# Kernel optimization log

Measured on AMD Instinct MI355X. Metric: run time of the kernel, lower is better.

## Reference

```python
import jax, jax.numpy as jnp
import numpy as np

# static config (levels=4, CDA=False branch -> self_attn_4, scale=4, f=False)
SHAPES = [(80, 80), (40, 40), (20, 20), (10, 10)]
D = 256; NH = 8; NL = 4; NP = 4; DFF = 1024; DH = D // NH
L = sum(h * w for h, w in SHAPES)  # 8500
B = 1


def layer_norm(x, g, b, eps=1e-5):
    m = jnp.mean(x, axis=-1, keepdims=True)
    v = jnp.mean((x - m) ** 2, axis=-1, keepdims=True)
    return (x - m) * jax.lax.rsqrt(v + eps) * g + b


def ms_deform_attn_core(value, loc, attn):
    # value: [B, L, NH, DH]; loc: [B, Lq, NH, NL, NP, 2] in [0,1]; attn: [B, Lq, NH, NL, NP]
    Bq, Lq = loc.shape[0], loc.shape[1]
    out = jnp.zeros((Bq, NH, Lq, DH), value.dtype)
    start = 0
    for lvl, (Hl, Wl) in enumerate(SHAPES):
        v = value[:, start:start + Hl * Wl]          # [B, HW, NH, DH]
        start += Hl * Wl
        v = v.transpose(0, 2, 1, 3)                  # [B, NH, HW, DH]
        ll = loc[:, :, :, lvl]                       # [B, Lq, NH, NP, 2]
        # grid_sample semantics: align_corners=False, padding_mode='zeros'
        x = ll[..., 0] * Wl - 0.5
        y = ll[..., 1] * Hl - 0.5
        x0 = jnp.floor(x); y0 = jnp.floor(y)
        acc = jnp.zeros((Bq, NH, Lq, NP, DH), value.dtype)
        for dy in (0, 1):
            for dx in (0, 1):
                xi = x0 + dx; yi = y0 + dy
                w = (1.0 - jnp.abs(x - xi)) * (1.0 - jnp.abs(y - yi))  # [B,Lq,NH,NP]
                valid = (xi >= 0) & (xi < Wl) & (yi >= 0) & (yi < Hl)
                xi_c = jnp.clip(xi, 0, Wl - 1).astype(jnp.int32)
                yi_c = jnp.clip(yi, 0, Hl - 1).astype(jnp.int32)
                lin = (yi_c * Wl + xi_c).transpose(0, 2, 1, 3).reshape(Bq, NH, Lq * NP)
                g = jnp.take_along_axis(v, lin[..., None], axis=2).reshape(Bq, NH, Lq, NP, DH)
                wv = (w * valid.astype(w.dtype)).transpose(0, 2, 1, 3)[..., None]
                acc = acc + g * wv
        aw = attn[:, :, :, lvl].transpose(0, 2, 1, 3)[..., None]  # [B,NH,Lq,NP,1]
        out = out + jnp.sum(acc * aw, axis=3)
    return out.transpose(0, 2, 1, 3).reshape(Bq, Lq, NH * DH)


def setup_inputs():
    key = jax.random.key(0)
    ks = jax.random.split(key, 24)
    s = 0.02
    d = {}
    d['src'] = jax.random.normal(ks[0], (B, L, D), jnp.float32)
    d['pos'] = jax.random.normal(ks[1], (B, L, D), jnp.float32)
    d['reference_points'] = jax.random.uniform(ks[2], (B, L, NL, 2), jnp.float32)
    d['spatial_shapes'] = jnp.array(SHAPES, jnp.int32)
    d['level_start_index'] = jnp.array(np.cumsum([0] + [h * w for h, w in SHAPES[:-1]]), jnp.int32)
    d['scale'] = 4
    # MSDeformAttn params
    d['Wo'] = jax.random.normal(ks[3], (D, NH * NL * NP * 2), jnp.float32) * s
    d['bo'] = jax.random.normal(ks[4], (NH * NL * NP * 2,), jnp.float32) * s
    d['Wa'] = jax.random.normal(ks[5], (D, NH * NL * NP), jnp.float32) * s
    d['ba'] = jax.random.normal(ks[6], (NH * NL * NP,), jnp.float32) * s
    d['Wv'] = jax.random.normal(ks[7], (D, D), jnp.float32) * s
    d['bv'] = jnp.zeros((D,), jnp.float32)
    d['Wout'] = jax.random.normal(ks[8], (D, D), jnp.float32) * s
    d['bout'] = jnp.zeros((D,), jnp.float32)
    # FFN + LayerNorms
    d['W1'] = jax.random.normal(ks[9], (D, DFF), jnp.float32) * s
    d['b1'] = jnp.zeros((DFF,), jnp.float32)
    d['W2'] = jax.random.normal(ks[10], (DFF, D), jnp.float32) * s
    d['b2'] = jnp.zeros((D,), jnp.float32)
    d['g1'] = jnp.ones((D,), jnp.float32); d['be1'] = jnp.zeros((D,), jnp.float32)
    d['g2'] = jnp.ones((D,), jnp.float32); d['be2'] = jnp.zeros((D,), jnp.float32)
    return d


def reference(src, pos, reference_points, spatial_shapes, level_start_index, scale,
              Wo, bo, Wa, ba, Wv, bv, Wout, bout, W1, b1, W2, b2, g1, be1, g2, be2):
    Bq, Lq, _ = src.shape
    q = src + pos  # with_pos_embed
    # sampling offsets & attention weights (softmax over levels*points)
    off = (q @ Wo + bo).reshape(Bq, Lq, NH, NL, NP, 2)
    attn = jax.nn.softmax((q @ Wa + ba).reshape(Bq, Lq, NH, NL * NP), axis=-1)
    attn = attn.reshape(Bq, Lq, NH, NL, NP)
    value = (src @ Wv + bv).reshape(Bq, L, NH, DH)
    # offset normalizer is (W, H) per level
    normalizer = jnp.stack([spatial_shapes[:, 1], spatial_shapes[:, 0]], -1).astype(src.dtype)
    loc = reference_points[:, :, None, :, None, :] + off / normalizer[None, None, None, :, None, :]
    src2 = ms_deform_attn_core(value, loc, attn) @ Wout + bout
    # residual + norm1 (dropout = eval identity)
    x = layer_norm(src + src2, g1, be1)
    # FFN
    ffn = jax.nn.relu(x @ W1 + b1) @ W2 + b2
    x = layer_norm(x + ffn, g2, be2)
    return x
```

## Files before the change

kernel.cpp:

```cpp
#include <hip/hip_runtime.h>
#include <hip/hip_bf16.h>
#include <string.h>

#define D 256
#define NH 8
#define DH 32
#define NL 4
#define NP 4
#define DFF 1024
#define LTOT 8500

typedef __bf16 bf16x8 __attribute__((ext_vector_type(8)));
typedef float floatx4 __attribute__((ext_vector_type(4)));

__device__ inline unsigned bpack(float a, float b) {
    __hip_bfloat16 ha = __float2bfloat16(a), hb = __float2bfloat16(b);
    unsigned short ua, ub;
    memcpy(&ua, &ha, 2); memcpy(&ub, &hb, 2);
    return (unsigned)ua | ((unsigned)ub << 16);
}

__device__ inline void gload16(const void* g, void* l) {
    __builtin_amdgcn_global_load_lds((const __attribute__((address_space(1))) void*)g,
                                     (__attribute__((address_space(3))) void*)l,
                                     16, 0, 0);
}

__global__ void transpose_all(const float* W0, const float* W1_, const float* W2_,
                              const float* W3, const float* W4, const float* W5,
                              __hip_bfloat16* T0, __hip_bfloat16* T1, __hip_bfloat16* T2,
                              __hip_bfloat16* T3, __hip_bfloat16* T4, __hip_bfloat16* T5,
                              const float* src, const float* pos,
                              __hip_bfloat16* qb, __hip_bfloat16* srcb) {
    int id = blockIdx.x;
    if (id >= 736) {
        int idx = (id - 736) * 2048 + threadIdx.x * 8;
        if (idx < LTOT * 256) {
            float4 s0 = *(const float4*)(src + idx);
            float4 s1 = *(const float4*)(src + idx + 4);
            float4 p0 = *(const float4*)(pos + idx);
            float4 p1 = *(const float4*)(pos + idx + 4);
            uint4 us, uq;
            us.x = bpack(s0.x, s0.y); us.y = bpack(s0.z, s0.w);
            us.z = bpack(s1.x, s1.y); us.w = bpack(s1.z, s1.w);
            uq.x = bpack(s0.x + p0.x, s0.y + p0.y); uq.y = bpack(s0.z + p0.z, s0.w + p0.w);
            uq.z = bpack(s1.x + p1.x, s1.y + p1.y); uq.w = bpack(s1.z + p1.z, s1.w + p1.w);
            *(uint4*)(srcb + idx) = us;
            *(uint4*)(qb + idx)  = uq;
        }
        return;
    }
    const int cum[7] = {0, 64, 96, 160, 224, 480, 736};
    int mi = 0;
    while (id >= cum[mi + 1]) mi++;
    int lid = id - cum[mi];
    const float* W; __hip_bfloat16* T; int K, N;
    switch (mi) {
        case 0: W = W0; T = T0; K = 256;  N = 256;  break;
        case 1: W = W1_; T = T1; K = 256; N = 128;  break;
        case 2: W = W2_; T = T2; K = 256; N = 256;  break;
        case 3: W = W3; T = T3; K = 256;  N = 256;  break;
        case 4: W = W4; T = T4; K = 256;  N = 1024; break;
        default: W = W5; T = T5; K = 1024; N = 256; break;
    }
    int ntx = N >> 5;
    int n0 = (lid % ntx) * 32, k0 = (lid / ntx) * 32;
    __shared__ float t[32][33];
    int tx = threadIdx.x & 31, ty = threadIdx.x >> 5;
#pragma unroll
    for (int i = 0; i < 32; i += 8)
        t[ty + i][tx] = W[(size_t)(k0 + ty + i) * N + n0 + tx];
    __syncthreads();
#pragma unroll
    for (int i = 0; i < 32; i += 8)
        T[(size_t)(n0 + ty + i) * K + k0 + tx] = __float2bfloat16(t[tx][ty + i]);
}

__global__ __launch_bounds__(256) void proj2(
    const __hip_bfloat16* __restrict__ qb, const __hip_bfloat16* __restrict__ srcb,
    const __hip_bfloat16* __restrict__ WoT, const __hip_bfloat16* __restrict__ WaT,
    const __hip_bfloat16* __restrict__ WvT,
    const float* __restrict__ bo, const float* __restrict__ ba, const float* __restrict__ bv,
    float* __restrict__ locb, float* __restrict__ attnb, __hip_bfloat16* __restrict__ valb,
    int M) {
    constexpr int BM = 64, BN = 64, BK = 64, K = 256;
    __shared__ __align__(16) __hip_bfloat16 sA[BM * BK];
    __shared__ __align__(16) __hip_bfloat16 sB[BN * BK];

    int n0 = blockIdx.x * BN;
    int m0 = blockIdx.y * BM;

    const __hip_bfloat16* BT;
    const __hip_bfloat16* A;
    const float* bias;
    int ncol0, Nout;
    float* Cf; __hip_bfloat16* Cb;
    if (n0 < 256)      { A = qb;   BT = WoT; bias = bo; ncol0 = n0;       Nout = 256; Cf = locb;  Cb = nullptr; }
    else if (n0 < 384) { A = qb;   BT = WaT; bias = ba; ncol0 = n0 - 256; Nout = 128; Cf = attnb; Cb = nullptr; }
    else               { A = srcb; BT = WvT; bias = bv; ncol0 = n0 - 384; Nout = 256; Cf = nullptr; Cb = valb; }

    int tid = threadIdx.x, wave = tid >> 6, lane = tid & 63;
    int wm = (wave >> 1) * 32, wn = (wave & 1) * 32;

    floatx4 acc[2][2];
#pragma unroll
    for (int i = 0; i < 2; i++)
#pragma unroll
        for (int j = 0; j < 2; j++)
#pragma unroll
            for (int e = 0; e < 4; e++) acc[i][j][e] = 0.f;

    int lrow = lane & 15, swz = lrow & 7;
    int scol = ((lane & 7) ^ (lane >> 3)) << 3;

    const __hip_bfloat16* aP[2];
    const __hip_bfloat16* bP[2];
#pragma unroll
    for (int i = 0; i < 2; i++) {
        int ra = m0 + i * 32 + wave * 8 + (lane >> 3); if (ra >= M) ra = M - 1;
        aP[i] = A + (size_t)ra * K + scol;
        int rb = ncol0 + i * 32 + wave * 8 + (lane >> 3);
        bP[i] = BT + (size_t)rb * K + scol;
    }
    int dOff = wave * 1024 + lane * 16;

    for (int k0 = 0; k0 < K; k0 += BK) {
#pragma unroll
        for (int i = 0; i < 2; i++) gload16(aP[i] + k0, (char*)sA + i * 4096 + dOff);
#pragma unroll
        for (int i = 0; i < 2; i++) gload16(bP[i] + k0, (char*)sB + i * 4096 + dOff);
        __syncthreads();
#pragma unroll
        for (int kk = 0; kk < 2; kk++) {
            int co = (((kk << 2) + (lane >> 4)) ^ swz) << 3;
            bf16x8 af[2], bfr[2];
#pragma unroll
            for (int tm = 0; tm < 2; tm++)
                af[tm] = *(const bf16x8*)(&sA[(wm + tm * 16 + lrow) * BK + co]);
#pragma unroll
            for (int tn = 0; tn < 2; tn++)
                bfr[tn] = *(const bf16x8*)(&sB[(wn + tn * 16 + lrow) * BK + co]);
#pragma unroll
            for (int tm = 0; tm < 2; tm++)
#pragma unroll
                for (int tn = 0; tn < 2; tn++)
                    acc[tm][tn] = __builtin_amdgcn_mfma_f32_16x16x32_bf16(af[tm], bfr[tn], acc[tm][tn], 0, 0, 0);
        }
        __syncthreads();
    }

    int lcol = lane & 15, lr4 = (lane >> 4) * 4;
#pragma unroll
    for (int tm = 0; tm < 2; tm++) {
#pragma unroll
        for (int i = 0; i < 4; i++) {
            int row = m0 + wm + tm * 16 + lr4 + i;
            if (row < M) {
#pragma unroll
                for (int tn = 0; tn < 2; tn++) {
                    int col = ncol0 + wn + tn * 16 + lcol;
                    float v = acc[tm][tn][i] + bias[col];
                    if (Cf) Cf[(size_t)row * Nout + col] = v;
                    else    Cb[(size_t)row * Nout + col] = __float2bfloat16(v);
                }
            }
        }
    }
}

__global__ __launch_bounds__(256) void deform(const __hip_bfloat16* __restrict__ value,
                                              const float* __restrict__ locraw,
                                              const float* __restrict__ logits,
                                              const float* __restrict__ refp,
                                              __hip_bfloat16* __restrict__ out) {
    __shared__ float wS[4][8][16][4];
    __shared__ int   aS[4][8][16][4];
    int tid = threadIdx.x;
    int q0 = blockIdx.x * 4;

    {
        int sub = tid >> 6, h = (tid >> 3) & 7, t8 = tid & 7;
        int q = q0 + sub;
        const float* lg = logits + q * 128 + h * 16;
        float l0 = lg[t8], l1 = lg[t8 + 8];
        float mx = fmaxf(l0, l1);
#pragma unroll
        for (int m = 1; m < 8; m <<= 1) mx = fmaxf(mx, __shfl_xor(mx, m, 64));
        float e0 = __expf(l0 - mx), e1 = __expf(l1 - mx);
        float s = e0 + e1;
#pragma unroll
        for (int m = 1; m < 8; m <<= 1) s += __shfl_xor(s, m, 64);
        float inv = 1.f / s;

        const int starts[4] = {0, 6400, 8000, 8400};
#pragma unroll
        for (int j = 0; j < 2; j++) {
            int pp = t8 + 8 * j;
            float a = (j ? e1 : e0) * inv;
            int l = pp >> 2;
            int Wl = 80 >> l;
            float nv = (float)Wl;
            float rx = refp[q * 8 + l * 2 + 0];
            float ry = refp[q * 8 + l * 2 + 1];
            float lx = rx + locraw[q * 256 + h * 32 + pp * 2 + 0] / nv;
            float ly = ry + locraw[q * 256 + h * 32 + pp * 2 + 1] / nv;
            float x = lx * nv - 0.5f;
            float y = ly * nv - 0.5f;
            float x0f = floorf(x), y0f = floorf(y);
            float fx = x - x0f, fy = y - y0f;
            int x0 = (int)x0f, y0 = (int)y0f;
            float wts[4] = {(1.f - fx) * (1.f - fy), fx * (1.f - fy),
                            (1.f - fx) * fy,         fx * fy};
            int st = starts[l];
#pragma unroll
            for (int t = 0; t < 4; t++) {
                int xi = x0 + (t & 1), yi = y0 + (t >> 1);
                bool valid = (xi >= 0) & (xi < Wl) & (yi >= 0) & (yi < Wl);
                int xc = min(max(xi, 0), Wl - 1), yc = min(max(yi, 0), Wl - 1);
                wS[sub][h][pp][t] = valid ? wts[t] * a : 0.f;
                aS[sub][h][pp][t] = (st + yc * Wl + xc) * 512 + h * 64;
            }
        }
    }
    __syncthreads();

    int sub = tid >> 6, h = (tid >> 3) & 7, l8 = tid & 7;
    int q = q0 + sub;
    const char* vb = (const char*)value;
    int lo = l8 * 8;
    float a0 = 0.f, a1 = 0.f, a2 = 0.f, a3 = 0.f;
#pragma unroll
    for (int p = 0; p < 16; p++) {
        floatx4 w = *(const floatx4*)&wS[sub][h][p][0];
        int4 av = *(const int4*)&aS[sub][h][p][0];
#pragma unroll
        for (int t = 0; t < 4; t++) {
            int ad = (t == 0) ? av.x : (t == 1) ? av.y : (t == 2) ? av.z : av.w;
            uint2 u = *(const uint2*)(vb + ad + lo);
            float wt = w[t];
            a0 += wt * __uint_as_float(u.x << 16);
            a1 += wt * __uint_as_float(u.x & 0xffff0000u);
            a2 += wt * __uint_as_float(u.y << 16);
            a3 += wt * __uint_as_float(u.y & 0xffff0000u);
        }
    }
    uint2 o;
    o.x = bpack(a0, a1);
    o.y = bpack(a2, a3);
    *(uint2*)((char*)out + q * 512 + h * 64 + l8 * 8) = o;
}

__global__ __launch_bounds__(512) void tail(
    const __hip_bfloat16* __restrict__ aob,
    const __hip_bfloat16* __restrict__ WoutT, const float* __restrict__ bout,
    const float* __restrict__ src,
    const float* __restrict__ g1, const float* __restrict__ be1,
    const __hip_bfloat16* __restrict__ W1T, const float* __restrict__ b1,
    const __hip_bfloat16* __restrict__ W2T, const float* __restrict__ b2,
    const float* __restrict__ g2, const float* __restrict__ be2,
    float* __restrict__ outf, int M) {
    __shared__ __align__(16) __hip_bfloat16 sAx[16 * 256];
    __shared__ __align__(16) __hip_bfloat16 H[16 * 1032];
    __shared__ __align__(16) __hip_bfloat16 sB[256 * 64];
    __shared__ float psum[8][16], psq[8][16], mS[16], rS[16];

    int tid = threadIdx.x, wave = tid >> 6, lane = tid & 63;
    int m0 = blockIdx.x * 16;
    int lrow = lane & 15, swz = lrow & 7, q2 = lane >> 4;
    int quad = lane >> 4, lcol = lane & 15;
    int swzA = (lrow & 7) << 3;
    int scolB = ((tid & 7) ^ ((tid >> 3) & 7)) << 3;

    {
        int rr = tid >> 5, cc = tid & 31;
        int gr = m0 + rr; if (gr >= M) gr = M - 1;
        int colel = (cc * 8) ^ ((rr & 7) << 3);
        gload16(aob + (size_t)gr * 256 + colel, (char*)sAx + tid * 16);
    }

    const __hip_bfloat16* bP[4];
#pragma unroll
    for (int i = 0; i < 4; i++)
        bP[i] = WoutT + (size_t)(i * 64 + (tid >> 3)) * 256 + scolB;

    floatx4 acc[2];
#pragma unroll
    for (int j = 0; j < 2; j++)
#pragma unroll
        for (int e = 0; e < 4; e++) acc[j][e] = 0.f;

    for (int t = 0; t < 4; t++) {
#pragma unroll
        for (int i = 0; i < 4; i++) gload16(bP[i] + t * 64, (char*)sB + i * 8192 + tid * 16);
        __syncthreads();
#pragma unroll
        for (int kk = 0; kk < 2; kk++) {
            int co = (((kk << 2) + q2) ^ swz) << 3;
            bf16x8 af = *(const bf16x8*)(&sAx[lrow * 256 + ((t * 64 + kk * 32 + q2 * 8) ^ swzA)]);
            bf16x8 bfr[2];
#pragma unroll
            for (int tn = 0; tn < 2; tn++)
                bfr[tn] = *(const bf16x8*)(&sB[(wave * 32 + tn * 16 + lrow) * 64 + co]);
#pragma unroll
            for (int tn = 0; tn < 2; tn++)
                acc[tn] = __builtin_amdgcn_mfma_f32_16x16x32_bf16(af, bfr[tn], acc[tn], 0, 0, 0);
        }
        __syncthreads();
    }

    float v1[2][4];
#pragma unroll
    for (int i = 0; i < 4; i++) {
        int row = quad * 4 + i;
        int grow = m0 + row; if (grow >= M) grow = M - 1;
#pragma unroll
        for (int tn = 0; tn < 2; tn++) {
            int col = wave * 32 + tn * 16 + lcol;
            v1[tn][i] = acc[tn][i] + bout[col] + src[(size_t)grow * 256 + col];
        }
    }
#pragma unroll
    for (int i = 0; i < 4; i++) {
        float s = 0.f, s2 = 0.f;
#pragma unroll
        for (int tn = 0; tn < 2; tn++) { float x = v1[tn][i]; s += x; s2 += x * x; }
#pragma unroll
        for (int m = 1; m < 16; m <<= 1) {
            s  += __shfl_xor(s, m, 64);
            s2 += __shfl_xor(s2, m, 64);
        }
        if (lcol == 0) { int row = quad * 4 + i; psum[wave][row] = s; psq[wave][row] = s2; }
    }
    __syncthreads();
    if (tid < 16) {
        float s = 0.f, s2 = 0.f;
#pragma unroll
        for (int w = 0; w < 8; w++) { s += psum[w][tid]; s2 += psq[w][tid]; }
        float m = s * (1.f / 256.f);
        float var = fmaxf(s2 * (1.f / 256.f) - m * m, 0.f);
        mS[tid] = m; rS[tid] = rsqrtf(var + 1e-5f);
    }
    __syncthreads();

    float x1r[2][4];
#pragma unroll
    for (int i = 0; i < 4; i++) {
        int row = quad * 4 + i;
        float m = mS[row], r = rS[row];
#pragma unroll
        for (int tn = 0; tn < 2; tn++) {
            int col = wave * 32 + tn * 16 + lcol;
            float o = (v1[tn][i] - m) * r * g1[col] + be1[col];
            x1r[tn][i] = o;
            sAx[row * 256 + (col ^ ((row & 7) << 3))] = __float2bfloat16(o);
        }
    }

    for (int c = 0; c < 4; c++) {
        const __hip_bfloat16* bPc[4];
#pragma unroll
        for (int i = 0; i < 4; i++)
            bPc[i] = W1T + (size_t)(c * 256 + i * 64 + (tid >> 3)) * 256 + scolB;

        floatx4 accA[2];
#pragma unroll
        for (int j = 0; j < 2; j++)
#pragma unroll
            for (int e = 0; e < 4; e++) accA[j][e] = 0.f;

        for (int t = 0; t < 4; t++) {
#pragma unroll
            for (int i = 0; i < 4; i++) gload16(bPc[i] + t * 64, (char*)sB + i * 8192 + tid * 16);
            __syncthreads();
#pragma unroll
            for (int kk = 0; kk < 2; kk++) {
                int co = (((kk << 2) + q2) ^ swz) << 3;
                bf16x8 af = *(const bf16x8*)(&sAx[lrow * 256 + ((t * 64 + kk * 32 + q2 * 8) ^ swzA)]);
                bf16x8 bfr[2];
#pragma unroll
                for (int tn = 0; tn < 2; tn++)
                    bfr[tn] = *(const bf16x8*)(&sB[(wave * 32 + tn * 16 + lrow) * 64 + co]);
#pragma unroll
                for (int tn = 0; tn < 2; tn++)
                    accA[tn] = __builtin_amdgcn_mfma_f32_16x16x32_bf16(af, bfr[tn], accA[tn], 0, 0, 0);
            }
            __syncthreads();
        }

#pragma unroll
        for (int i = 0; i < 4; i++) {
            int row = quad * 4 + i;
#pragma unroll
            for (int tn = 0; tn < 2; tn++) {
                int col = c * 256 + wave * 32 + tn * 16 + lcol;
                float v = accA[tn][i] + b1[col];
                H[row * 1032 + col] = __float2bfloat16(fmaxf(v, 0.f));
            }
        }
    }

    const __hip_bfloat16* bP2[4];
#pragma unroll
    for (int i = 0; i < 4; i++)
        bP2[i] = W2T + (size_t)(i * 64 + (tid >> 3)) * 1024 + scolB;

    floatx4 acc2[2];
#pragma unroll
    for (int j = 0; j < 2; j++)
#pragma unroll
        for (int e = 0; e < 4; e++) acc2[j][e] = 0.f;

    for (int t = 0; t < 16; t++) {
#pragma unroll
        for (int i = 0; i < 4; i++) gload16(bP2[i] + t * 64, (char*)sB + i * 8192 + tid * 16);
        __syncthreads();
#pragma unroll
        for (int kk = 0; kk < 2; kk++) {
            int co = (((kk << 2) + q2) ^ swz) << 3;
            bf16x8 af = *(const bf16x8*)(&H[lrow * 1032 + t * 64 + kk * 32 + q2 * 8]);
            bf16x8 bfr[2];
#pragma unroll
            for (int tn = 0; tn < 2; tn++)
                bfr[tn] = *(const bf16x8*)(&sB[(wave * 32 + tn * 16 + lrow) * 64 + co]);
#pragma unroll
            for (int tn = 0; tn < 2; tn++)
                acc2[tn] = __builtin_amdgcn_mfma_f32_16x16x32_bf16(af, bfr[tn], acc2[tn], 0, 0, 0);
        }
        __syncthreads();
    }

    float v2[2][4];
#pragma unroll
    for (int i = 0; i < 4; i++) {
#pragma unroll
        for (int tn = 0; tn < 2; tn++) {
            int col = wave * 32 + tn * 16 + lcol;
            v2[tn][i] = acc2[tn][i] + b2[col] + x1r[tn][i];
        }
    }
#pragma unroll
    for (int i = 0; i < 4; i++) {
        float s = 0.f, s2 = 0.f;
#pragma unroll
        for (int tn = 0; tn < 2; tn++) { float x = v2[tn][i]; s += x; s2 += x * x; }
#pragma unroll
        for (int m = 1; m < 16; m <<= 1) {
            s  += __shfl_xor(s, m, 64);
            s2 += __shfl_xor(s2, m, 64);
        }
        if (lcol == 0) { int row = quad * 4 + i; psum[wave][row] = s; psq[wave][row] = s2; }
    }
    __syncthreads();
    if (tid < 16) {
        float s = 0.f, s2 = 0.f;
#pragma unroll
        for (int w = 0; w < 8; w++) { s += psum[w][tid]; s2 += psq[w][tid]; }
        float m = s * (1.f / 256.f);
        float var = fmaxf(s2 * (1.f / 256.f) - m * m, 0.f);
        mS[tid] = m; rS[tid] = rsqrtf(var + 1e-5f);
    }
    __syncthreads();

#pragma unroll
    for (int i = 0; i < 4; i++) {
        int row = quad * 4 + i;
        int grow = m0 + row;
        if (grow < M) {
            float m = mS[row], r = rS[row];
#pragma unroll
            for (int tn = 0; tn < 2; tn++) {
                int col = wave * 32 + tn * 16 + lcol;
                outf[(size_t)grow * 256 + col] = (v2[tn][i] - m) * r * g2[col] + be2[col];
            }
        }
    }
}

extern "C" void kernel_launch(void* const* d_in, const int* in_sizes, int n_in,
                              void* d_out, int out_size, void* d_ws, size_t ws_size,
                              hipStream_t stream) {
    const float* src  = (const float*)d_in[0];
    const float* pos  = (const float*)d_in[1];
    const float* refp = (const float*)d_in[2];
    const float* Wo   = (const float*)d_in[6];
    const float* bo   = (const float*)d_in[7];
    const float* Wa   = (const float*)d_in[8];
    const float* ba   = (const float*)d_in[9];
    const float* Wv   = (const float*)d_in[10];
    const float* bv   = (const float*)d_in[11];
    const float* Wout = (const float*)d_in[12];
    const float* bout = (const float*)d_in[13];
    const float* W1   = (const float*)d_in[14];
    const float* b1   = (const float*)d_in[15];
    const float* W2   = (const float*)d_in[16];
    const float* b2   = (const float*)d_in[17];
    const float* g1   = (const float*)d_in[18];
    const float* be1  = (const float*)d_in[19];
    const float* g2   = (const float*)d_in[20];
    const float* be2  = (const float*)d_in[21];
    float* out = (float*)d_out;
    char* ws = (char*)d_ws;

    __hip_bfloat16* WoT   = (__hip_bfloat16*)(ws + 0);
    __hip_bfloat16* WaT   = (__hip_bfloat16*)(ws + 131072);
    __hip_bfloat16* WvT   = (__hip_bfloat16*)(ws + 196608);
    __hip_bfloat16* WoutT = (__hip_bfloat16*)(ws + 327680);
    __hip_bfloat16* W1T   = (__hip_bfloat16*)(ws + 458752);
    __hip_bfloat16* W2T   = (__hip_bfloat16*)(ws + 983040);
    float*          locb  = (float*)(ws + 1507328);
    float*          attnb = (float*)(ws + 10211328);
    __hip_bfloat16* valb  = (__hip_bfloat16*)(ws + 14563328);
    __hip_bfloat16* aob   = (__hip_bfloat16*)(ws + 18915328);
    __hip_bfloat16* qb    = (__hip_bfloat16*)(ws + 23267328);
    __hip_bfloat16* srcb  = (__hip_bfloat16*)(ws + 27619328);

    transpose_all<<<736 + 1063, 256, 0, stream>>>(Wo, Wa, Wv, Wout, W1, W2,
                                                  WoT, WaT, WvT, WoutT, W1T, W2T,
                                                  src, pos, qb, srcb);

    proj2<<<dim3(10, 133), 256, 0, stream>>>(qb, srcb, WoT, WaT, WvT, bo, ba, bv,
                                             locb, attnb, valb, LTOT);

    deform<<<2125, 256, 0, stream>>>(valb, locb, attnb, refp, aob);

    tail<<<532, 512, 0, stream>>>(aob, WoutT, bout, src, g1, be1,
                                  W1T, b1, W2T, b2, g2, be2, out, LTOT);
}
```

Before: 197.7 us.

## Defer tail weight transposes into deform kernel and widen proj2 K tile

The transposes of Wout, W1 and W2 move out of the first prep kernel and become 576 extra blocks appended to the deform kernel. This shortens the critical path before proj2 and lets that work overlap with the memory-bound gather. proj2 also doubles its K tile to 128 with a new 16-way XOR swizzle, halving the number of K iterations and barriers at the cost of doubled LDS per block. Deform now uses a 32KB shared buffer, which could lower occupancy for the gather blocks.

```diff
diff --git a/kernel.cpp b/kernel.cpp
--- a/kernel.cpp
+++ b/kernel.cpp
@@ -26,54 +26,48 @@
                                      16, 0, 0);
 }
 
-__global__ void transpose_all(const float* W0, const float* W1_, const float* W2_,
-                              const float* W3, const float* W4, const float* W5,
-                              __hip_bfloat16* T0, __hip_bfloat16* T1, __hip_bfloat16* T2,
-                              __hip_bfloat16* T3, __hip_bfloat16* T4, __hip_bfloat16* T5,
-                              const float* src, const float* pos,
-                              __hip_bfloat16* qb, __hip_bfloat16* srcb) {
+__device__ inline void wtile(const float* W, __hip_bfloat16* T, int K, int N,
+                             int n0, int k0, float* t ) {
+    int tx = threadIdx.x & 31, ty = threadIdx.x >> 5;
+#pragma unroll
+    for (int i = 0; i < 32; i += 8)
+        t[(ty + i) * 33 + tx] = W[(size_t)(k0 + ty + i) * N + n0 + tx];
+    __syncthreads();
+#pragma unroll
+    for (int i = 0; i < 32; i += 8)
+        T[(size_t)(n0 + ty + i) * K + k0 + tx] = __float2bfloat16(t[tx * 33 + ty + i]);
+    __syncthreads();
+}
+
+__global__ void prep3(const float* Wo, const float* Wa, const float* Wv,
+                      __hip_bfloat16* WoT, __hip_bfloat16* WaT, __hip_bfloat16* WvT,
+                      const float* src, const float* pos,
+                      __hip_bfloat16* qb, __hip_bfloat16* srcb) {
+    __shared__ float t[32 * 33];
     int id = blockIdx.x;
-    if (id >= 736) {
-        int idx = (id - 736) * 2048 + threadIdx.x * 8;
-        if (idx < LTOT * 256) {
-            float4 s0 = *(const float4*)(src + idx);
-            float4 s1 = *(const float4*)(src + idx + 4);
-            float4 p0 = *(const float4*)(pos + idx);
-            float4 p1 = *(const float4*)(pos + idx + 4);
-            uint4 us, uq;
-            us.x = bpack(s0.x, s0.y); us.y = bpack(s0.z, s0.w);
-            us.z = bpack(s1.x, s1.y); us.w = bpack(s1.z, s1.w);
-            uq.x = bpack(s0.x + p0.x, s0.y + p0.y); uq.y = bpack(s0.z + p0.z, s0.w + p0.w);
-            uq.z = bpack(s1.x + p1.x, s1.y + p1.y); uq.w = bpack(s1.z + p1.z, s1.w + p1.w);
-            *(uint4*)(srcb + idx) = us;
-            *(uint4*)(qb + idx)  = uq;
-        }
+    if (id < 160) {
+        const float* W; __hip_bfloat16* T; int K, N, lid;
+        if (id < 64)       { W = Wo; T = WoT; K = 256; N = 256; lid = id; }
+        else if (id < 96)  { W = Wa; T = WaT; K = 256; N = 128; lid = id - 64; }
+        else               { W = Wv; T = WvT; K = 256; N = 256; lid = id - 96; }
+        int ntx = N >> 5;
+        wtile(W, T, K, N, (lid % ntx) * 32, (lid / ntx) * 32, t);
         return;
     }
-    const int cum[7] = {0, 64, 96, 160, 224, 480, 736};
-    int mi = 0;
-    while (id >= cum[mi + 1]) mi++;
-    int lid = id - cum[mi];
-    const float* W; __hip_bfloat16* T; int K, N;
-    switch (mi) {
-        case 0: W = W0; T = T0; K = 256;  N = 256;  break;
-        case 1: W = W1_; T = T1; K = 256; N = 128;  break;
-        case 2: W = W2_; T = T2; K = 256; N = 256;  break;
-        case 3: W = W3; T = T3; K = 256;  N = 256;  break;
-        case 4: W = W4; T = T4; K = 256;  N = 1024; break;
-        default: W = W5; T = T5; K = 1024; N = 256; break;
-    }
-    int ntx = N >> 5;
-    int n0 = (lid % ntx) * 32, k0 = (lid / ntx) * 32;
-    __shared__ float t[32][33];
-    int tx = threadIdx.x & 31, ty = threadIdx.x >> 5;
-#pragma unroll
-    for (int i = 0; i < 32; i += 8)
-        t[ty + i][tx] = W[(size_t)(k0 + ty + i) * N + n0 + tx];
-    __syncthreads();
-#pragma unroll
-    for (int i = 0; i < 32; i += 8)
-        T[(size_t)(n0 + ty + i) * K + k0 + tx] = __float2bfloat16(t[tx][ty + i]);
+    int idx = (id - 160) * 2048 + threadIdx.x * 8;
+    if (idx < LTOT * 256) {
+        float4 s0 = *(const float4*)(src + idx);
+        float4 s1 = *(const float4*)(src + idx + 4);
+        float4 p0 = *(const float4*)(pos + idx);
+        float4 p1 = *(const float4*)(pos + idx + 4);
+        uint4 us, uq;
+        us.x = bpack(s0.x, s0.y); us.y = bpack(s0.z, s0.w);
+        us.z = bpack(s1.x, s1.y); us.w = bpack(s1.z, s1.w);
+        uq.x = bpack(s0.x + p0.x, s0.y + p0.y); uq.y = bpack(s0.z + p0.z, s0.w + p0.w);
+        uq.z = bpack(s1.x + p1.x, s1.y + p1.y); uq.w = bpack(s1.z + p1.z, s1.w + p1.w);
+        *(uint4*)(srcb + idx) = us;
+        *(uint4*)(qb + idx)  = uq;
+    }
 }
 
 __global__ __launch_bounds__(256) void proj2(
@@ -83,7 +77,7 @@
     const float* __restrict__ bo, const float* __restrict__ ba, const float* __restrict__ bv,
     float* __restrict__ locb, float* __restrict__ attnb, __hip_bfloat16* __restrict__ valb,
     int M) {
-    constexpr int BM = 64, BN = 64, BK = 64, K = 256;
+    constexpr int BM = 64, BN = 64, BK = 128, K = 256;
     __shared__ __align__(16) __hip_bfloat16 sA[BM * BK];
     __shared__ __align__(16) __hip_bfloat16 sB[BN * BK];
 
@@ -110,29 +104,29 @@
 #pragma unroll
             for (int e = 0; e < 4; e++) acc[i][j][e] = 0.f;
 
-    int lrow = lane & 15, swz = lrow & 7;
-    int scol = ((lane & 7) ^ (lane >> 3)) << 3;
-
-    const __hip_bfloat16* aP[2];
-    const __hip_bfloat16* bP[2];
-#pragma unroll
-    for (int i = 0; i < 2; i++) {
-        int ra = m0 + i * 32 + wave * 8 + (lane >> 3); if (ra >= M) ra = M - 1;
+    int lrow = lane & 15, q2 = lane >> 4;
+
+    const __hip_bfloat16* aP[4];
+    const __hip_bfloat16* bP[4];
+#pragma unroll
+    for (int i = 0; i < 4; i++) {
+        int ci = i * 256 + tid;
+        int row = ci >> 4, cc = ci & 15;
+        int scol = ((cc ^ (row & 15)) << 3);
+        int ra = m0 + row; if (ra >= M) ra = M - 1;
         aP[i] = A + (size_t)ra * K + scol;
-        int rb = ncol0 + i * 32 + wave * 8 + (lane >> 3);
-        bP[i] = BT + (size_t)rb * K + scol;
-    }
-    int dOff = wave * 1024 + lane * 16;
+        bP[i] = BT + (size_t)(ncol0 + row) * K + scol;
+    }
 
     for (int k0 = 0; k0 < K; k0 += BK) {
 #pragma unroll
-        for (int i = 0; i < 2; i++) gload16(aP[i] + k0, (char*)sA + i * 4096 + dOff);
-#pragma unroll
-        for (int i = 0; i < 2; i++) gload16(bP[i] + k0, (char*)sB + i * 4096 + dOff);
+        for (int i = 0; i < 4; i++) gload16(aP[i] + k0, (char*)sA + (i * 256 + tid) * 16);
+#pragma unroll
+        for (int i = 0; i < 4; i++) gload16(bP[i] + k0, (char*)sB + (i * 256 + tid) * 16);
         __syncthreads();
 #pragma unroll
-        for (int kk = 0; kk < 2; kk++) {
-            int co = (((kk << 2) + (lane >> 4)) ^ swz) << 3;
+        for (int kk = 0; kk < 4; kk++) {
+            int co = (((kk << 2) + q2) ^ lrow) << 3;
             bf16x8 af[2], bfr[2];
 #pragma unroll
             for (int tm = 0; tm < 2; tm++)
@@ -168,15 +162,32 @@
     }
 }
 
-__global__ __launch_bounds__(256) void deform(const __hip_bfloat16* __restrict__ value,
-                                              const float* __restrict__ locraw,
-                                              const float* __restrict__ logits,
-                                              const float* __restrict__ refp,
-                                              __hip_bfloat16* __restrict__ out) {
-    __shared__ float wS[4][8][16][4];
-    __shared__ int   aS[4][8][16][4];
+__global__ __launch_bounds__(256) void deform2(
+    const __hip_bfloat16* __restrict__ value,
+    const float* __restrict__ locraw,
+    const float* __restrict__ logits,
+    const float* __restrict__ refp,
+    __hip_bfloat16* __restrict__ out,
+    const float* Wout, const float* W1, const float* W2,
+    __hip_bfloat16* WoutT, __hip_bfloat16* W1T, __hip_bfloat16* W2T) {
+    __shared__ __align__(16) char dsm[32768];
     int tid = threadIdx.x;
-    int q0 = blockIdx.x * 4;
+    int bid = blockIdx.x;
+
+    if (bid >= 2125) {
+        int id = bid - 2125;
+        const float* W; __hip_bfloat16* T; int K, N, lid;
+        if (id < 64)       { W = Wout; T = WoutT; K = 256;  N = 256;  lid = id; }
+        else if (id < 320) { W = W1;   T = W1T;   K = 256;  N = 1024; lid = id - 64; }
+        else               { W = W2;   T = W2T;   K = 1024; N = 256;  lid = id - 320; }
+        int ntx = N >> 5;
+        wtile(W, T, K, N, (lid % ntx) * 32, (lid / ntx) * 32, (float*)dsm);
+        return;
+    }
+
+    float* wS = (float*)dsm;
+    int*   aS = (int*)(dsm + 8192);
+    int q0 = bid * 4;
 
     {
         int sub = tid >> 6, h = (tid >> 3) & 7, t8 = tid & 7;
@@ -217,8 +228,9 @@
                 int xi = x0 + (t & 1), yi = y0 + (t >> 1);
                 bool valid = (xi >= 0) & (xi < Wl) & (yi >= 0) & (yi < Wl);
                 int xc = min(max(xi, 0), Wl - 1), yc = min(max(yi, 0), Wl - 1);
-                wS[sub][h][pp][t] = valid ? wts[t] * a : 0.f;
-                aS[sub][h][pp][t] = (st + yc * Wl + xc) * 512 + h * 64;
+                int base = ((sub * 8 + h) * 16 + pp) * 4 + t;
+                wS[base] = valid ? wts[t] * a : 0.f;
+                aS[base] = (st + yc * Wl + xc) * 512 + h * 64;
             }
         }
     }
@@ -231,8 +243,9 @@
     float a0 = 0.f, a1 = 0.f, a2 = 0.f, a3 = 0.f;
 #pragma unroll
     for (int p = 0; p < 16; p++) {
-        floatx4 w = *(const floatx4*)&wS[sub][h][p][0];
-        int4 av = *(const int4*)&aS[sub][h][p][0];
+        int base = ((sub * 8 + h) * 16 + p) * 4;
+        floatx4 w = *(const floatx4*)&wS[base];
+        int4 av = *(const int4*)&aS[base];
 #pragma unroll
         for (int t = 0; t < 4; t++) {
             int ad = (t == 0) ? av.x : (t == 1) ? av.y : (t == 2) ? av.z : av.w;
@@ -514,14 +527,14 @@
     __hip_bfloat16* qb    = (__hip_bfloat16*)(ws + 23267328);
     __hip_bfloat16* srcb  = (__hip_bfloat16*)(ws + 27619328);
 
-    transpose_all<<<736 + 1063, 256, 0, stream>>>(Wo, Wa, Wv, Wout, W1, W2,
-                                                  WoT, WaT, WvT, WoutT, W1T, W2T,
-                                                  src, pos, qb, srcb);
+    prep3<<<160 + 1063, 256, 0, stream>>>(Wo, Wa, Wv, WoT, WaT, WvT,
+                                          src, pos, qb, srcb);
 
     proj2<<<dim3(10, 133), 256, 0, stream>>>(qb, srcb, WoT, WaT, WvT, bo, ba, bv,
                                              locb, attnb, valb, LTOT);
 
-    deform<<<2125, 256, 0, stream>>>(valb, locb, attnb, refp, aob);
+    deform2<<<2125 + 576, 256, 0, stream>>>(valb, locb, attnb, refp, aob,
+                                            Wout, W1, W2, WoutT, W1T, W2T);
 
     tail<<<532, 512, 0, stream>>>(aob, WoutT, bout, src, g1, be1,
                                   W1T, b1, W2T, b2, g2, be2, out, LTOT);
```

Result: no change. 196.5 us (-0.6%).
